# Kernel tuning notes

Hardware: AMD Instinct MI355X
Metric: run time of the kernel (lower is better)

Reference implementation:

```python
import jax, jax.numpy as jnp
import numpy as np

EPS_COS = 1e-8   # torch F.cosine_similarity eps
EPS_L1 = 1e-12   # torch F.normalize eps


def setup_inputs() -> dict:
    key = jax.random.key(0)
    k1, k2, k3, k4 = jax.random.split(key, 4)
    B, D, C = 32768, 768, 200
    features = jax.random.normal(k1, (B, D), dtype=jnp.float32)
    centers = jax.random.normal(k2, (C, D), dtype=jnp.float32)
    labels = jax.random.randint(k3, (B,), 0, C)
    labelled_or_not = jax.random.randint(k4, (B,), 0, 2).astype(jnp.bool_)
    return {"features": features, "centers": centers, "labels": labels,
            "labelled_or_not": labelled_or_not}


def reference(features, centers, labels, labelled_or_not):
    # cosine similarity: x.y / (max(|x|,eps) * max(|y|,eps))
    fn = features / jnp.maximum(jnp.linalg.norm(features, axis=1, keepdims=True), EPS_COS)
    cn = centers / jnp.maximum(jnp.linalg.norm(centers, axis=1, keepdims=True), EPS_COS)
    cos = jnp.einsum('bd,cd->bc', fn, cn)  # [B, C]

    # per-sample sign logic: label column -> +|cos|, all others -> -|cos|
    a = jnp.abs(cos)
    is_label = jax.nn.one_hot(labels, cos.shape[1], dtype=jnp.bool_)  # [B, C]
    signed = jnp.where(is_label, a, -a)

    # L1 normalize per row (||row||_1 == sum of |cos| regardless of signs)
    l1 = jnp.sum(a, axis=1, keepdims=True)
    normed = signed / jnp.maximum(l1, EPS_L1)

    # only labelled rows contribute (row-wise normalize is independent per row,
    # so masking after is equivalent to boolean-indexing before)
    contrib = jnp.where(labelled_or_not[:, None], normed, 0.0)
    return -jnp.sum(contrib)
```

## Files before the change

kernel.cpp:

```cpp
#include <hip/hip_runtime.h>
#include <hip/hip_bf16.h>

#define NROWS 32768
#define DIMS  768
#define NC    200
#define CPAD  256
#define KSTEP 32
#define NSTEP (DIMS / KSTEP)
#define ROWSB 64

typedef __attribute__((ext_vector_type(8))) short short8;
typedef __attribute__((ext_vector_type(4))) float f32x4;

__device__ __forceinline__ unsigned pk_bf16(float lo, float hi) {
  union { __hip_bfloat162 h; unsigned u; } c;
  c.h = __float22bfloat162_rn(make_float2(lo, hi));
  return c.u;
}

__global__ __launch_bounds__(256) void prep_centers_k(const float* __restrict__ centers,
                                                      short* __restrict__ cnb2,
                                                      float* __restrict__ out) {
  const int c = blockIdx.x;
  const int tid = threadIdx.x;
  if (c == 0 && tid == 0) out[0] = 0.f;
  if (c >= NC) {
    for (int d = tid; d < DIMS; d += 256)
      cnb2[(d >> 5) * (CPAD * KSTEP) + c * KSTEP + (d & 31)] = 0;
    return;
  }
  float ssq = 0.f;
  for (int d = tid; d < DIMS; d += 256) {
    float v = centers[c * DIMS + d];
    ssq += v * v;
  }
#pragma unroll
  for (int off = 32; off > 0; off >>= 1) ssq += __shfl_down(ssq, off);
  __shared__ float red[4];
  const int wid = tid >> 6, lane = tid & 63;
  if (lane == 0) red[wid] = ssq;
  __syncthreads();
  const float tot = red[0] + red[1] + red[2] + red[3];
  const float inv = 1.f / fmaxf(sqrtf(tot), 1e-8f);
  for (int d = tid; d < DIMS; d += 256) {
    const float v = centers[c * DIMS + d] * inv;
    union { __hip_bfloat16 h; short s; } cv;
    cv.h = __float2bfloat16(v);
    cnb2[(d >> 5) * (CPAD * KSTEP) + c * KSTEP + (d & 31)] = cv.s;
  }
}

__global__ __launch_bounds__(256) void cos_loss_k(
    const float* __restrict__ feats,
    const short* __restrict__ cnb2,
    const int* __restrict__ labels,
    const int* __restrict__ labelled,
    float* __restrict__ out) {
  const int tid = threadIdx.x;
  const int w = tid >> 6;
  const int lane = tid & 63;
  const int m = lane & 15;
  const int kg = lane >> 4;
  const int swzf = (m >> 1) & 3;
  const int rowBase = blockIdx.x * ROWSB;

  __shared__ short As[2][ROWSB][32];
  __shared__ short Bs[2][CPAD][32];
  __shared__ float invs[ROWSB];
  __shared__ int   labLds[ROWSB];
  __shared__ int   lblLds[ROWSB];
  __shared__ float l1part[4][ROWSB];
  __shared__ float alpart[4][ROWSB];

  if (tid < ROWSB) {
    labLds[tid] = labels[rowBase + tid];
    lblLds[tid] = labelled[rowBase + tid];
  }

  const int arow = tid >> 2;
  const int akg  = tid & 3;
  const int aswz = (arow >> 1) & 3;
  const float* asrc = feats + (size_t)(rowBase + arow) * DIMS + akg * 8;
  short* adst0 = &As[0][arow][(akg ^ aswz) * 8];
  short* adst1 = &As[1][arow][(akg ^ aswz) * 8];
  const int bcol = tid;
  const int bswz = (bcol >> 1) & 3;
  const short* bsrc = cnb2 + bcol * KSTEP;

  f32x4 acc[4][4];
#pragma unroll
  for (int mi = 0; mi < 4; ++mi)
#pragma unroll
    for (int ni = 0; ni < 4; ++ni) acc[mi][ni] = (f32x4){0.f, 0.f, 0.f, 0.f};

  float ssq = 0.f;

  {
    const float4 va = *(const float4*)(asrc);
    const float4 vb = *(const float4*)(asrc + 4);
    ssq += va.x*va.x + va.y*va.y + va.z*va.z + va.w*va.w;
    ssq += vb.x*vb.x + vb.y*vb.y + vb.z*vb.z + vb.w*vb.w;
    union { short8 s; unsigned u[4]; } p;
    p.u[0] = pk_bf16(va.x, va.y); p.u[1] = pk_bf16(va.z, va.w);
    p.u[2] = pk_bf16(vb.x, vb.y); p.u[3] = pk_bf16(vb.z, vb.w);
    *(short8*)adst0 = p.s;
    const short8 b0 = *(const short8*)(bsrc + 0);
    const short8 b1 = *(const short8*)(bsrc + 8);
    const short8 b2 = *(const short8*)(bsrc + 16);
    const short8 b3 = *(const short8*)(bsrc + 24);
    *(short8*)(&Bs[0][bcol][((0 ^ bswz)) * 8]) = b0;
    *(short8*)(&Bs[0][bcol][((1 ^ bswz)) * 8]) = b1;
    *(short8*)(&Bs[0][bcol][((2 ^ bswz)) * 8]) = b2;
    *(short8*)(&Bs[0][bcol][((3 ^ bswz)) * 8]) = b3;
  }
  __syncthreads();

#pragma unroll 2
  for (int ks = 0; ks < NSTEP; ++ks) {
    const int cur = ks & 1, nxt = cur ^ 1;
    float4 va, vb;
    short8 b0, b1, b2, b3;
    if (ks < NSTEP - 1) {
      const float* ap = asrc + (ks + 1) * KSTEP;
      va = *(const float4*)(ap);
      vb = *(const float4*)(ap + 4);
      const short* bp = bsrc + (size_t)(ks + 1) * (CPAD * KSTEP);
      b0 = *(const short8*)(bp + 0);
      b1 = *(const short8*)(bp + 8);
      b2 = *(const short8*)(bp + 16);
      b3 = *(const short8*)(bp + 24);
    }
    {
      short8 af[4], bf[4];
#pragma unroll
      for (int mi = 0; mi < 4; ++mi)
        af[mi] = *(const short8*)(&As[cur][mi * 16 + m][((kg ^ swzf)) * 8]);
#pragma unroll
      for (int ni = 0; ni < 4; ++ni)
        bf[ni] = *(const short8*)(&Bs[cur][w * 64 + ni * 16 + m][((kg ^ swzf)) * 8]);
#pragma unroll
      for (int mi = 0; mi < 4; ++mi)
#pragma unroll
        for (int ni = 0; ni < 4; ++ni)
          acc[mi][ni] = __builtin_amdgcn_mfma_f32_16x16x32_bf16(af[mi], bf[ni], acc[mi][ni], 0, 0, 0);
    }
    if (ks < NSTEP - 1) {
      ssq += va.x*va.x + va.y*va.y + va.z*va.z + va.w*va.w;
      ssq += vb.x*vb.x + vb.y*vb.y + vb.z*vb.z + vb.w*vb.w;
      union { short8 s; unsigned u[4]; } p;
      p.u[0] = pk_bf16(va.x, va.y); p.u[1] = pk_bf16(va.z, va.w);
      p.u[2] = pk_bf16(vb.x, vb.y); p.u[3] = pk_bf16(vb.z, vb.w);
      *(short8*)(nxt ? adst1 : adst0) = p.s;
      *(short8*)(&Bs[nxt][bcol][((0 ^ bswz)) * 8]) = b0;
      *(short8*)(&Bs[nxt][bcol][((1 ^ bswz)) * 8]) = b1;
      *(short8*)(&Bs[nxt][bcol][((2 ^ bswz)) * 8]) = b2;
      *(short8*)(&Bs[nxt][bcol][((3 ^ bswz)) * 8]) = b3;
    }
    __syncthreads();
  }

  ssq += __shfl_xor(ssq, 1);
  ssq += __shfl_xor(ssq, 2);
  if ((tid & 3) == 0) invs[arow] = 1.f / fmaxf(sqrtf(ssq), 1e-8f);
  __syncthreads();

#pragma unroll
  for (int mi = 0; mi < 4; ++mi) {
    float l1r[4] = {0.f, 0.f, 0.f, 0.f};
    float alr[4] = {0.f, 0.f, 0.f, 0.f};
    float iv[4];
    int labr[4];
#pragma unroll
    for (int r = 0; r < 4; ++r) {
      const int row = mi * 16 + kg * 4 + r;
      iv[r] = invs[row];
      labr[r] = labLds[row];
    }
#pragma unroll
    for (int ni = 0; ni < 4; ++ni) {
      const int col = w * 64 + ni * 16 + m;
#pragma unroll
      for (int r = 0; r < 4; ++r) {
        const float a = fabsf(acc[mi][ni][r] * iv[r]);
        l1r[r] += a;
        if (col == labr[r]) alr[r] += a;
      }
    }
#pragma unroll
    for (int r = 0; r < 4; ++r) {
#pragma unroll
      for (int off = 1; off < 16; off <<= 1) {
        l1r[r] += __shfl_xor(l1r[r], off);
        alr[r] += __shfl_xor(alr[r], off);
      }
    }
    if (m == 0) {
#pragma unroll
      for (int r = 0; r < 4; ++r) {
        l1part[w][mi * 16 + kg * 4 + r] = l1r[r];
        alpart[w][mi * 16 + kg * 4 + r] = alr[r];
      }
    }
  }
  __syncthreads();

  if (tid < ROWSB) {
    const float L = l1part[0][tid] + l1part[1][tid] + l1part[2][tid] + l1part[3][tid];
    const float A = alpart[0][tid] + alpart[1][tid] + alpart[2][tid] + alpart[3][tid];
    float c = lblLds[tid] ? (L - 2.f * A) / fmaxf(L, 1e-12f) : 0.f;
#pragma unroll
    for (int off = 1; off < 64; off <<= 1) c += __shfl_xor(c, off);
    if (tid == 0) atomicAdd(out, c);
  }
}

extern "C" void kernel_launch(void* const* d_in, const int* in_sizes, int n_in,
                              void* d_out, int out_size, void* d_ws, size_t ws_size,
                              hipStream_t stream) {
  const float* feats = (const float*)d_in[0];
  const float* centers = (const float*)d_in[1];
  const int* labels = (const int*)d_in[2];
  const int* labelled = (const int*)d_in[3];
  float* out = (float*)d_out;
  short* cnb2 = (short*)d_ws;

  prep_centers_k<<<CPAD, 256, 0, stream>>>(centers, cnb2, out);
  cos_loss_k<<<NROWS / ROWSB, 256, 0, stream>>>(feats, cnb2, labels, labelled, out);
}
```

Measured before the change: 38.01 us.

## Deepen K-loop prefetch to two register slots with explicit double buffering

Restructures the main K loop so global loads are issued two steps ahead into two register slots, while LDS writes for the next buffer and MFMA compute on the current buffer are interleaved inside a manually unrolled two-step body. The aim is to hide more global memory latency behind MFMA work. The cost is roughly double the prefetch register pressure, which could lower occupancy.

```diff
diff --git a/kernel.cpp b/kernel.cpp
--- a/kernel.cpp
+++ b/kernel.cpp
@@ -81,8 +81,6 @@
   const int akg  = tid & 3;
   const int aswz = (arow >> 1) & 3;
   const float* asrc = feats + (size_t)(rowBase + arow) * DIMS + akg * 8;
-  short* adst0 = &As[0][arow][(akg ^ aswz) * 8];
-  short* adst1 = &As[1][arow][(akg ^ aswz) * 8];
   const int bcol = tid;
   const int bswz = (bcol >> 1) & 3;
   const short* bsrc = cnb2 + bcol * KSTEP;
@@ -95,69 +93,72 @@
 
   float ssq = 0.f;
 
-  {
-    const float4 va = *(const float4*)(asrc);
-    const float4 vb = *(const float4*)(asrc + 4);
-    ssq += va.x*va.x + va.y*va.y + va.z*va.z + va.w*va.w;
-    ssq += vb.x*vb.x + vb.y*vb.y + vb.z*vb.z + vb.w*vb.w;
-    union { short8 s; unsigned u[4]; } p;
-    p.u[0] = pk_bf16(va.x, va.y); p.u[1] = pk_bf16(va.z, va.w);
-    p.u[2] = pk_bf16(vb.x, vb.y); p.u[3] = pk_bf16(vb.z, vb.w);
-    *(short8*)adst0 = p.s;
-    const short8 b0 = *(const short8*)(bsrc + 0);
-    const short8 b1 = *(const short8*)(bsrc + 8);
-    const short8 b2 = *(const short8*)(bsrc + 16);
-    const short8 b3 = *(const short8*)(bsrc + 24);
-    *(short8*)(&Bs[0][bcol][((0 ^ bswz)) * 8]) = b0;
-    *(short8*)(&Bs[0][bcol][((1 ^ bswz)) * 8]) = b1;
-    *(short8*)(&Bs[0][bcol][((2 ^ bswz)) * 8]) = b2;
-    *(short8*)(&Bs[0][bcol][((3 ^ bswz)) * 8]) = b3;
-  }
-  __syncthreads();
-
-#pragma unroll 2
-  for (int ks = 0; ks < NSTEP; ++ks) {
-    const int cur = ks & 1, nxt = cur ^ 1;
-    float4 va, vb;
-    short8 b0, b1, b2, b3;
-    if (ks < NSTEP - 1) {
-      const float* ap = asrc + (ks + 1) * KSTEP;
-      va = *(const float4*)(ap);
-      vb = *(const float4*)(ap + 4);
-      const short* bp = bsrc + (size_t)(ks + 1) * (CPAD * KSTEP);
-      b0 = *(const short8*)(bp + 0);
-      b1 = *(const short8*)(bp + 8);
-      b2 = *(const short8*)(bp + 16);
-      b3 = *(const short8*)(bp + 24);
-    }
-    {
-      short8 af[4], bf[4];
-#pragma unroll
-      for (int mi = 0; mi < 4; ++mi)
-        af[mi] = *(const short8*)(&As[cur][mi * 16 + m][((kg ^ swzf)) * 8]);
-#pragma unroll
-      for (int ni = 0; ni < 4; ++ni)
-        bf[ni] = *(const short8*)(&Bs[cur][w * 64 + ni * 16 + m][((kg ^ swzf)) * 8]);
-#pragma unroll
-      for (int mi = 0; mi < 4; ++mi)
-#pragma unroll
-        for (int ni = 0; ni < 4; ++ni)
-          acc[mi][ni] = __builtin_amdgcn_mfma_f32_16x16x32_bf16(af[mi], bf[ni], acc[mi][ni], 0, 0, 0);
-    }
-    if (ks < NSTEP - 1) {
-      ssq += va.x*va.x + va.y*va.y + va.z*va.z + va.w*va.w;
-      ssq += vb.x*vb.x + vb.y*vb.y + vb.z*vb.z + vb.w*vb.w;
-      union { short8 s; unsigned u[4]; } p;
-      p.u[0] = pk_bf16(va.x, va.y); p.u[1] = pk_bf16(va.z, va.w);
-      p.u[2] = pk_bf16(vb.x, vb.y); p.u[3] = pk_bf16(vb.z, vb.w);
-      *(short8*)(nxt ? adst1 : adst0) = p.s;
-      *(short8*)(&Bs[nxt][bcol][((0 ^ bswz)) * 8]) = b0;
-      *(short8*)(&Bs[nxt][bcol][((1 ^ bswz)) * 8]) = b1;
-      *(short8*)(&Bs[nxt][bcol][((2 ^ bswz)) * 8]) = b2;
-      *(short8*)(&Bs[nxt][bcol][((3 ^ bswz)) * 8]) = b3;
-    }
+  float4 S0_alo, S0_ahi; short8 S0_b0, S0_b1, S0_b2, S0_b3;
+  float4 S1_alo, S1_ahi; short8 S1_b0, S1_b1, S1_b2, S1_b3;
+
+#define LOAD_SLOT(P, step) do {                                          \
+    const float* ap_ = asrc + (step) * KSTEP;                            \
+    P##_alo = *(const float4*)(ap_);                                     \
+    P##_ahi = *(const float4*)(ap_ + 4);                                 \
+    const short* bp_ = bsrc + (size_t)(step) * (CPAD * KSTEP);           \
+    P##_b0 = *(const short8*)(bp_ + 0);                                  \
+    P##_b1 = *(const short8*)(bp_ + 8);                                  \
+    P##_b2 = *(const short8*)(bp_ + 16);                                 \
+    P##_b3 = *(const short8*)(bp_ + 24);                                 \
+  } while (0)
+
+#define WRITE_SLOT(P, buf) do {                                          \
+    ssq += P##_alo.x*P##_alo.x + P##_alo.y*P##_alo.y                     \
+         + P##_alo.z*P##_alo.z + P##_alo.w*P##_alo.w;                    \
+    ssq += P##_ahi.x*P##_ahi.x + P##_ahi.y*P##_ahi.y                     \
+         + P##_ahi.z*P##_ahi.z + P##_ahi.w*P##_ahi.w;                    \
+    union { short8 s; unsigned u[4]; } p_;                               \
+    p_.u[0] = pk_bf16(P##_alo.x, P##_alo.y);                             \
+    p_.u[1] = pk_bf16(P##_alo.z, P##_alo.w);                             \
+    p_.u[2] = pk_bf16(P##_ahi.x, P##_ahi.y);                             \
+    p_.u[3] = pk_bf16(P##_ahi.z, P##_ahi.w);                             \
+    *(short8*)(&As[(buf)][arow][(akg ^ aswz) * 8]) = p_.s;               \
+    *(short8*)(&Bs[(buf)][bcol][(0 ^ bswz) * 8]) = P##_b0;               \
+    *(short8*)(&Bs[(buf)][bcol][(1 ^ bswz) * 8]) = P##_b1;               \
+    *(short8*)(&Bs[(buf)][bcol][(2 ^ bswz) * 8]) = P##_b2;               \
+    *(short8*)(&Bs[(buf)][bcol][(3 ^ bswz) * 8]) = P##_b3;               \
+  } while (0)
+
+#define COMPUTE(buf) do {                                                \
+    short8 af[4], bf[4];                                                 \
+    _Pragma("unroll")                                                    \
+    for (int mi = 0; mi < 4; ++mi)                                       \
+      af[mi] = *(const short8*)(&As[(buf)][mi * 16 + m][(kg ^ swzf) * 8]); \
+    _Pragma("unroll")                                                    \
+    for (int ni = 0; ni < 4; ++ni)                                       \
+      bf[ni] = *(const short8*)(&Bs[(buf)][w * 64 + ni * 16 + m][(kg ^ swzf) * 8]); \
+    _Pragma("unroll")                                                    \
+    for (int mi = 0; mi < 4; ++mi)                                       \
+      _Pragma("unroll")                                                  \
+      for (int ni = 0; ni < 4; ++ni)                                     \
+        acc[mi][ni] = __builtin_amdgcn_mfma_f32_16x16x32_bf16(           \
+            af[mi], bf[ni], acc[mi][ni], 0, 0, 0);                       \
+  } while (0)
+
+  LOAD_SLOT(S0, 0);
+  WRITE_SLOT(S0, 0);
+  LOAD_SLOT(S1, 1);
+  __syncthreads();
+
+  for (int ks = 0; ks < NSTEP; ks += 2) {
+    if (ks + 2 < NSTEP) LOAD_SLOT(S0, ks + 2);
+    WRITE_SLOT(S1, 1);
+    COMPUTE(0);
     __syncthreads();
-  }
+    if (ks + 3 < NSTEP) LOAD_SLOT(S1, ks + 3);
+    if (ks + 2 < NSTEP) WRITE_SLOT(S0, 0);
+    COMPUTE(1);
+    __syncthreads();
+  }
+
+#undef LOAD_SLOT
+#undef WRITE_SLOT
+#undef COMPUTE
 
   ssq += __shfl_xor(ssq, 1);
   ssq += __shfl_xor(ssq, 2);
```

After: 38.41 us. No clear change (+1.0%).
